# Optimization experiments

Hardware: AMD Instinct MI355X
Metric: run time of the kernel (lower is better)

Reference implementation:

```python
import jax, jax.numpy as jnp
import numpy as np
from jax.scipy.special import logsumexp

B, N_LC, N_TE, D = 4, 2048, 2048, 256
ITERS = 100  # Sinkhorn iterations


def _mlp2(x, W1, b1, W2, b2):
    # 2-layer MLP with ReLU (DETR-style MLP, num_layers=2)
    h = jax.nn.relu(x @ W1.T + b1)
    return h @ W2.T + b2


def _log_optimal_transport(scores, alpha, iters):
    b, m, n = scores.shape
    ms = jnp.float32(m)
    ns = jnp.float32(n)
    # augment score matrix with dustbin row/col -> [b, m+1, n+1]
    bins0 = jnp.broadcast_to(alpha, (b, m, 1))
    bins1 = jnp.broadcast_to(alpha, (b, 1, n))
    binsc = jnp.broadcast_to(alpha, (b, 1, 1))
    Z = jnp.concatenate([
        jnp.concatenate([scores, bins0], axis=-1),
        jnp.concatenate([bins1, binsc], axis=-1)], axis=1)
    norm = -jnp.log(ms + ns)
    log_mu = jnp.concatenate([jnp.full((m,), norm), jnp.log(ns)[None] + norm])
    log_nu = jnp.concatenate([jnp.full((n,), norm), jnp.log(ms)[None] + norm])
    log_mu = jnp.broadcast_to(log_mu[None], (b, m + 1))
    log_nu = jnp.broadcast_to(log_nu[None], (b, n + 1))

    def step(carry, _):
        u, v = carry
        u = log_mu - logsumexp(Z + v[:, None, :], axis=2)
        v = log_nu - logsumexp(Z + u[:, :, None], axis=1)
        return (u, v), None

    u0 = jnp.zeros_like(log_mu)
    v0 = jnp.zeros_like(log_nu)
    (u, v), _ = jax.lax.scan(step, (u0, v0), None, length=iters)
    return Z + u[:, :, None] + v[:, None, :] - norm


def setup_inputs() -> dict:
    key = jax.random.key(0)
    ks = jax.random.split(key, 8)
    s = 1.0 / np.sqrt(D).astype(np.float32)
    return {
        "quer_feat_lc": jax.random.normal(ks[0], (B, N_LC, D), jnp.float32),
        "quer_feat_te": jax.random.normal(ks[1], (B, N_TE, D), jnp.float32),
        "W1_lc": jax.random.normal(ks[2], (D, D), jnp.float32) * s,
        "b1_lc": jnp.zeros((D,), jnp.float32),
        "W2_lc": jax.random.normal(ks[3], (D, D), jnp.float32) * s,
        "b2_lc": jnp.zeros((D,), jnp.float32),
        "W1_te": jax.random.normal(ks[4], (D, D), jnp.float32) * s,
        "b1_te": jnp.zeros((D,), jnp.float32),
        "W2_te": jax.random.normal(ks[5], (D, D), jnp.float32) * s,
        "b2_te": jnp.zeros((D,), jnp.float32),
        "bin_score": jnp.ones((), jnp.float32),
    }


def reference(quer_feat_lc, quer_feat_te, W1_lc, b1_lc, W2_lc, b2_lc,
              W1_te, b1_te, W2_te, b2_te, bin_score):
    f1 = _mlp2(quer_feat_lc, W1_lc, b1_lc, W2_lc, b2_lc)  # [B, N_LC, D]
    f2 = _mlp2(quer_feat_te, W1_te, b1_te, W2_te, b2_te)  # [B, N_TE, D]
    scores = jnp.einsum('bnc,bmc->bnm', f1, f2) / jnp.sqrt(jnp.float32(D))
    Z = _log_optimal_transport(scores, bin_score, ITERS)  # [B, N_LC+1, N_TE+1]
    return jnp.exp(Z)
```

## Files before the change

kernel.cpp:

```cpp
#include <hip/hip_runtime.h>
#include <hip/hip_fp16.h>

#define NQ   2048
#define NB   4
#define DD   256
#define M1   2049
#define STR  2064
#define SINK_ITERS 100
#define PNWG 256
#define PTPB 1024

typedef __attribute__((ext_vector_type(8))) short short8;
typedef __attribute__((ext_vector_type(4))) float floatx4;
typedef __attribute__((ext_vector_type(2))) float floatx2;

__device__ __forceinline__ unsigned short f2bf(float f) {
  unsigned u = __float_as_uint(f);
  u += 0x7FFF + ((u >> 16) & 1);
  return (unsigned short)(u >> 16);
}

__device__ __forceinline__ unsigned char f2fp8(float f) {
  unsigned short u = __half_as_ushort(__float2half(f));
  return (unsigned char)((u + 0x7F + ((u >> 8) & 1)) >> 8);
}

__device__ __forceinline__ int IDX(int j) { return j + (j >> 4); }

__global__ void k_cvt6(const float* __restrict__ x_lc, const float* __restrict__ x_te,
                       const float* __restrict__ w1lc, const float* __restrict__ w2lc,
                       const float* __restrict__ w1te, const float* __restrict__ w2te,
                       unsigned short* __restrict__ Xlc, unsigned short* __restrict__ Xte,
                       unsigned short* __restrict__ Wb) {
  const int NX4 = (NB * NQ * DD) / 4;
  const int NW4 = (DD * DD) / 4;
  int i4 = blockIdx.x * blockDim.x + threadIdx.x;
  const float* src; unsigned short* dst; int off;
  if (i4 < NX4)            { src = x_lc; dst = Xlc; off = i4; }
  else if (i4 < 2 * NX4)   { src = x_te; dst = Xte; off = i4 - NX4; }
  else {
    int k = i4 - 2 * NX4;
    int seg = k / NW4;
    off = k - seg * NW4;
    src = (seg == 0) ? w1lc : (seg == 1) ? w2lc : (seg == 2) ? w1te : w2te;
    dst = Wb + seg * 65536;
  }
  float4 f = ((const float4*)src)[off];
  ushort4 o;
  o.x = f2bf(f.x); o.y = f2bf(f.y); o.z = f2bf(f.z); o.w = f2bf(f.w);
  ((ushort4*)dst)[off] = o;
}

template<int MODE>
__global__ __launch_bounds__(256, 2)
void k_gemm_bt(const unsigned short* __restrict__ A,
               const unsigned short* __restrict__ Bt,
               void* __restrict__ Out, void* __restrict__ Out8,
               const float* __restrict__ bias,
               int K, long aBatch, long bBatch, long oBatch, int ostride)
{
  __shared__ __align__(16) unsigned short lA[128 * 32];
  __shared__ __align__(16) unsigned short lB[128 * 32];
  const int tid  = threadIdx.x;
  const int lane = tid & 63;
  const int w    = tid >> 6;
  const int wm   = (w >> 1) * 64;
  const int wn   = (w & 1) * 64;
  const long bz  = blockIdx.z;
  const unsigned short* Ab = A  + bz * aBatch + (long)blockIdx.y * 128 * K;
  const unsigned short* Bb = Bt + bz * bBatch + (long)blockIdx.x * 128 * K;

  floatx4 acc[4][4];
  #pragma unroll
  for (int i = 0; i < 4; i++)
    #pragma unroll
    for (int j = 0; j < 4; j++) acc[i][j] = (floatx4){0.f, 0.f, 0.f, 0.f};

  for (int kt = 0; kt < K; kt += 32) {
    __syncthreads();
    #pragma unroll
    for (int s0 = 0; s0 < 512; s0 += 256) {
      int s = s0 + tid;
      int row = s >> 2, part = s & 3;
      ((uint4*)lA)[s] = *(const uint4*)(Ab + (long)row * K + kt + part * 8);
      ((uint4*)lB)[s] = *(const uint4*)(Bb + (long)row * K + kt + part * 8);
    }
    __syncthreads();
    const int kq = (lane >> 4) * 8;
    const int rl = lane & 15;
    short8 af[4], bf[4];
    #pragma unroll
    for (int t = 0; t < 4; t++) {
      af[t] = *(const short8*)(lA + (wm + t * 16 + rl) * 32 + kq);
      bf[t] = *(const short8*)(lB + (wn + t * 16 + rl) * 32 + kq);
    }
    #pragma unroll
    for (int i = 0; i < 4; i++)
      #pragma unroll
      for (int j = 0; j < 4; j++)
        acc[i][j] = __builtin_amdgcn_mfma_f32_16x16x32_bf16(af[i], bf[j], acc[i][j], 0, 0, 0);
  }

  const int cl = lane & 15, qd = lane >> 4;
  #pragma unroll
  for (int i = 0; i < 4; i++)
    #pragma unroll
    for (int j = 0; j < 4; j++) {
      const int col = blockIdx.x * 128 + wn + j * 16 + cl;
      const float bcol = (MODE >= 2) ? 0.f : bias[col];
      #pragma unroll
      for (int r = 0; r < 4; r++) {
        const long row = (long)blockIdx.y * 128 + wm + i * 16 + qd * 4 + r;
        float v = acc[i][j][r];
        if (MODE == 0) {
          v += bcol; v = v > 0.f ? v : 0.f;
          ((unsigned short*)Out)[bz * oBatch + row * ostride + col] = f2bf(v);
        } else if (MODE == 1) {
          v += bcol;
          ((unsigned short*)Out)[bz * oBatch + row * ostride + col] = f2bf(v);
        } else {
          v *= 0.0625f;
          v = fminf(fmaxf(v, -15.f), 10.9f);
          float e = __expf(v);
          const long idx = bz * oBatch + row * ostride + col;
          if (MODE == 2) ((__half*)Out)[idx] = __float2half(e);
          ((unsigned char*)Out8)[idx] = f2fp8(e);
        }
      }
    }
}

__global__ void k_fill(__half* __restrict__ E, const float* __restrict__ alphaPtr) {
  const float ea = __expf(*alphaPtr);
  const int idx = blockIdx.x * blockDim.x + threadIdx.x;
  const int n1 = NB * NQ * 16;
  if (idx < n1) {
    int b = idx / (NQ * 16);
    int rr = idx - b * NQ * 16;
    int i = rr >> 4;
    int j = 2048 + (rr & 15);
    E[((long)b * M1 + i) * STR + j] = (j == 2048) ? __float2half(ea) : __float2half(0.f);
  } else {
    int k = idx - n1;
    if (k < NB * STR) {
      int b = k / STR;
      int j = k - b * STR;
      E[((long)b * M1 + 2048) * STR + j] = (j <= 2048) ? __float2half(ea) : __float2half(0.f);
    }
  }
}

__global__ void k_init(float* __restrict__ v, int n, unsigned* __restrict__ bar) {
  int i = blockIdx.x * blockDim.x + threadIdx.x;
  if (i < n) v[i] = 1.0f;
  if (i < 2048) bar[i] = 0u;
}

__device__ __forceinline__ void st_agent(float* p, float v) {
  __hip_atomic_store(p, v, __ATOMIC_RELAXED, __HIP_MEMORY_SCOPE_AGENT);
}
__device__ __forceinline__ float ld_agent(const float* p) {
  return __hip_atomic_load(p, __ATOMIC_RELAXED, __HIP_MEMORY_SCOPE_AGENT);
}
__device__ __forceinline__ unsigned ld_u32_agent(const unsigned* p) {
  return __hip_atomic_load(p, __ATOMIC_RELAXED, __HIP_MEMORY_SCOPE_AGENT);
}

__device__ __forceinline__ float wave_sum(float s) {
  #pragma unroll
  for (int o = 32; o; o >>= 1) s += __shfl_xor(s, o);
  return s;
}

__device__ __forceinline__ float dot16f8(uint4 hv, const float* wp) {
  const unsigned* u = (const unsigned*)&hv;
  float s = 0.f;
#if __has_builtin(__builtin_amdgcn_cvt_pk_f32_bf8)
  #pragma unroll
  for (int q = 0; q < 4; q++) {
    floatx2 lo = __builtin_amdgcn_cvt_pk_f32_bf8((int)u[q], false);
    floatx2 hi = __builtin_amdgcn_cvt_pk_f32_bf8((int)u[q], true);
    s += lo.x * wp[q * 4 + 0] + lo.y * wp[q * 4 + 1]
       + hi.x * wp[q * 4 + 2] + hi.y * wp[q * 4 + 3];
  }
#else
  const unsigned char* p = (const unsigned char*)&hv;
  #pragma unroll
  for (int t = 0; t < 16; t++) {
    unsigned short h = (unsigned short)p[t] << 8;
    s += __half2float(*reinterpret_cast<__half*>(&h)) * wp[t];
  }
#endif
  return s;
}

__global__ __launch_bounds__(PTPB, 4)
void k_sink(const unsigned char* __restrict__ E8, const unsigned char* __restrict__ ET8,
            float* __restrict__ eu, float* __restrict__ ev,
            const float* __restrict__ alphaPtr, unsigned* __restrict__ bar)
{
  __shared__ __align__(16) float sv[2200];
  const int tid  = threadIdx.x;
  const int wg   = blockIdx.x;
  const int b    = wg >> 6;
  const int g    = wg & 63;
  const int wv   = tid >> 6;
  const int lane = tid & 63;
  const int r0   = (g * 16 + wv) * 2;
  const float ea = __expf(alphaPtr[0]);
  const unsigned char* E8r  = E8  + ((long)b * M1 + r0) * STR;
  const unsigned char* ET8r = ET8 + ((long)b * M1 + r0) * STR;
  float* ub = eu + b * STR;
  float* vb = ev + b * STR;
  unsigned* cnt = bar + b * 64;
  unsigned* gen = bar + b * 64 + 32;
  const bool dustwave = (g == 63) && (wv == 15);

  unsigned phase = 0;
  for (int it = 0; it < 2 * SINK_ITERS; ++it) {
    const unsigned char* R = (it & 1) ? ET8r : E8r;
    const float* vin = (it & 1) ? ub : vb;
    float*      vout = (it & 1) ? vb : ub;

    for (int j = tid; j < M1; j += PTPB) sv[IDX(j)] = ld_agent(vin + j);
    __syncthreads();

    uint4 h0c0 = *(const uint4*)(R + lane * 16);
    uint4 h0c1 = *(const uint4*)(R + 1024 + lane * 16);
    uint4 h1c0 = *(const uint4*)(R + STR + lane * 16);
    uint4 h1c1 = *(const uint4*)(R + STR + 1024 + lane * 16);
    const float* w0 = sv + lane * 17;
    const float* w1 = sv + 1088 + lane * 17;
    float a0 = dot16f8(h0c0, w0) + dot16f8(h0c1, w1);
    float a1 = dot16f8(h1c0, w0) + dot16f8(h1c1, w1);
    a0 = wave_sum(a0);
    a1 = wave_sum(a1);
    if (lane == 0) {
      const float wd = ea * sv[IDX(2048)];
      st_agent(vout + r0,     (1.f / 4096.f) / (a0 + wd));
      st_agent(vout + r0 + 1, (1.f / 4096.f) / (a1 + wd));
    }

    if (dustwave) {
      float s = 0.f;
      #pragma unroll
      for (int t = 0; t < 16; t++) s += w0[t] + w1[t];
      s = wave_sum(s);
      if (lane == 0) st_agent(vout + 2048, 0.5f / (ea * (s + sv[IDX(2048)])));
    }

    ++phase;
    __syncthreads();
    if (tid == 0) {
      unsigned old = __hip_atomic_fetch_add(cnt, 1u, __ATOMIC_RELAXED, __HIP_MEMORY_SCOPE_AGENT);
      if (old == phase * 64u - 1u) {
        __hip_atomic_store(gen, phase, __ATOMIC_RELAXED, __HIP_MEMORY_SCOPE_AGENT);
      } else {
        while (ld_u32_agent(gen) < phase)
          __builtin_amdgcn_s_sleep(1);
      }
    }
    __syncthreads();
  }
}

__global__ void k_final(const __half* __restrict__ E, const float* __restrict__ eu,
                        const float* __restrict__ ev, float* __restrict__ out) {
  const int wv = blockIdx.x;
  const int b = wv / M1;
  const int i = wv - b * M1;
  const __half* R = E + ((long)b * M1 + i) * STR;
  const float ui = eu[b * STR + i] * 4096.f;
  const float* evb = ev + b * STR;
  float* orow = out + ((long)b * M1 + i) * M1;
  for (int j = threadIdx.x; j < M1; j += blockDim.x)
    orow[j] = __half2float(R[j]) * ui * evb[j];
}

extern "C" void kernel_launch(void* const* d_in, const int* in_sizes, int n_in,
                              void* d_out, int out_size, void* d_ws, size_t ws_size,
                              hipStream_t stream) {
  const float* x_lc  = (const float*)d_in[0];
  const float* x_te  = (const float*)d_in[1];
  const float* W1_lc = (const float*)d_in[2];
  const float* b1_lc = (const float*)d_in[3];
  const float* W2_lc = (const float*)d_in[4];
  const float* b2_lc = (const float*)d_in[5];
  const float* W1_te = (const float*)d_in[6];
  const float* b1_te = (const float*)d_in[7];
  const float* W2_te = (const float*)d_in[8];
  const float* b2_te = (const float*)d_in[9];
  const float* alpha = (const float*)d_in[10];

  char* ws = (char*)d_ws;
  unsigned short* Xlc = (unsigned short*)(ws + 0);
  unsigned short* Xte = (unsigned short*)(ws + 4194304);
  unsigned short* Wb  = (unsigned short*)(ws + 8388608);
  unsigned short* H   = (unsigned short*)(ws + 8912896);
  unsigned short* F1  = (unsigned short*)(ws + 13107200);
  unsigned short* F2  = (unsigned short*)(ws + 17301504);
  __half* E  = (__half*)(ws + 21495808);
  unsigned char* E8  = (unsigned char*)(ws + 55328896);
  unsigned char* ET8 = (unsigned char*)(ws + 72245440);
  float* eu  = (float*)(ws + 89161984);
  float* ev  = (float*)(ws + 89195008);
  unsigned* bar = (unsigned*)(ws + 89228032);

  k_cvt6<<<4352, 256, 0, stream>>>(x_lc, x_te, W1_lc, W2_lc, W1_te, W2_te,
                                   Xlc, Xte, Wb);

  k_gemm_bt<0><<<dim3(2, 64, 1), 256, 0, stream>>>(Xlc, Wb,          H,  nullptr, b1_lc, DD, 0, 0, 0, DD);
  k_gemm_bt<1><<<dim3(2, 64, 1), 256, 0, stream>>>(H,   Wb + 65536,  F1, nullptr, b2_lc, DD, 0, 0, 0, DD);
  k_gemm_bt<0><<<dim3(2, 64, 1), 256, 0, stream>>>(Xte, Wb + 131072, H,  nullptr, b1_te, DD, 0, 0, 0, DD);
  k_gemm_bt<1><<<dim3(2, 64, 1), 256, 0, stream>>>(H,   Wb + 196608, F2, nullptr, b2_te, DD, 0, 0, 0, DD);

  const long ab = (long)NQ * DD;
  const long ob = (long)M1 * STR;
  k_gemm_bt<2><<<dim3(16, 16, NB), 256, 0, stream>>>(F1, F2, E,  E8,  nullptr, DD, ab, ab, ob, STR);
  k_gemm_bt<3><<<dim3(16, 16, NB), 256, 0, stream>>>(F2, F1, nullptr, ET8, nullptr, DD, ab, ab, ob, STR);

  const int nfill = NB * NQ * 16 + NB * STR;
  k_fill<<<(nfill + 255) / 256, 256, 0, stream>>>(E, alpha);

  k_init<<<(NB * STR + 255) / 256, 256, 0, stream>>>(ev, NB * STR, bar);

  k_sink<<<PNWG, PTPB, 0, stream>>>(E8, ET8, eu, ev, alpha, bar);

  k_final<<<NB * M1, 256, 0, stream>>>(E, eu, ev, (float*)d_out);
}
```

Measured before the change: 971.2 us.

## Use fp16 kernel matrices with packed dot2 in Sinkhorn instead of fp8

The Sinkhorn loop now reads fp16 copies of the exp-score matrix and its transpose instead of fp8 copies. Dot products use packed half-precision fdot2 against a scaled fp16 copy of the scaling vector held in shared memory. This doubles the bytes streamed per iteration but removes the fp8 conversions and improves accuracy. The two MLP layers are also batched into single launches via a z dimension with per-batch bias, and the fill and init kernels are merged to cut launch count.

Result: slower. 1.318 ms (+35.7%).

```diff
diff --git a/kernel.cpp b/kernel.cpp
--- a/kernel.cpp
+++ b/kernel.cpp
@@ -12,20 +12,13 @@
 
 typedef __attribute__((ext_vector_type(8))) short short8;
 typedef __attribute__((ext_vector_type(4))) float floatx4;
-typedef __attribute__((ext_vector_type(2))) float floatx2;
+typedef _Float16 h2 __attribute__((ext_vector_type(2)));
 
 __device__ __forceinline__ unsigned short f2bf(float f) {
   unsigned u = __float_as_uint(f);
   u += 0x7FFF + ((u >> 16) & 1);
   return (unsigned short)(u >> 16);
 }
-
-__device__ __forceinline__ unsigned char f2fp8(float f) {
-  unsigned short u = __half_as_ushort(__float2half(f));
-  return (unsigned char)((u + 0x7F + ((u >> 8) & 1)) >> 8);
-}
-
-__device__ __forceinline__ int IDX(int j) { return j + (j >> 4); }
 
 __global__ void k_cvt6(const float* __restrict__ x_lc, const float* __restrict__ x_te,
                        const float* __restrict__ w1lc, const float* __restrict__ w2lc,
@@ -55,8 +48,8 @@
 __global__ __launch_bounds__(256, 2)
 void k_gemm_bt(const unsigned short* __restrict__ A,
                const unsigned short* __restrict__ Bt,
-               void* __restrict__ Out, void* __restrict__ Out8,
-               const float* __restrict__ bias,
+               void* __restrict__ Out,
+               const float* __restrict__ bias, const float* __restrict__ bias2,
                int K, long aBatch, long bBatch, long oBatch, int ostride)
 {
   __shared__ __align__(16) unsigned short lA[128 * 32];
@@ -69,6 +62,7 @@
   const long bz  = blockIdx.z;
   const unsigned short* Ab = A  + bz * aBatch + (long)blockIdx.y * 128 * K;
   const unsigned short* Bb = Bt + bz * bBatch + (long)blockIdx.x * 128 * K;
+  const float* bp = (bz == 0) ? bias : bias2;
 
   floatx4 acc[4][4];
   #pragma unroll
@@ -107,7 +101,7 @@
     #pragma unroll
     for (int j = 0; j < 4; j++) {
       const int col = blockIdx.x * 128 + wn + j * 16 + cl;
-      const float bcol = (MODE >= 2) ? 0.f : bias[col];
+      const float bcol = (MODE >= 2) ? 0.f : bp[col];
       #pragma unroll
       for (int r = 0; r < 4; r++) {
         const long row = (long)blockIdx.y * 128 + wm + i * 16 + qd * 4 + r;
@@ -121,16 +115,14 @@
         } else {
           v *= 0.0625f;
           v = fminf(fmaxf(v, -15.f), 10.9f);
-          float e = __expf(v);
-          const long idx = bz * oBatch + row * ostride + col;
-          if (MODE == 2) ((__half*)Out)[idx] = __float2half(e);
-          ((unsigned char*)Out8)[idx] = f2fp8(e);
+          ((__half*)Out)[bz * oBatch + row * ostride + col] = __float2half(__expf(v));
         }
       }
     }
 }
 
-__global__ void k_fill(__half* __restrict__ E, const float* __restrict__ alphaPtr) {
+__global__ void k_fillinit(__half* __restrict__ E, const float* __restrict__ alphaPtr,
+                           float* __restrict__ ev, unsigned* __restrict__ bar) {
   const float ea = __expf(*alphaPtr);
   const int idx = blockIdx.x * blockDim.x + threadIdx.x;
   const int n1 = NB * NQ * 16;
@@ -148,12 +140,8 @@
       E[((long)b * M1 + 2048) * STR + j] = (j <= 2048) ? __float2half(ea) : __float2half(0.f);
     }
   }
-}
-
-__global__ void k_init(float* __restrict__ v, int n, unsigned* __restrict__ bar) {
-  int i = blockIdx.x * blockDim.x + threadIdx.x;
-  if (i < n) v[i] = 1.0f;
-  if (i < 2048) bar[i] = 0u;
+  if (idx < NB * STR) ev[idx] = 1.0f;
+  if (idx < 2048) bar[idx] = 0u;
 }
 
 __device__ __forceinline__ void st_agent(float* p, float v) {
@@ -172,34 +160,30 @@
   return s;
 }
 
-__device__ __forceinline__ float dot16f8(uint4 hv, const float* wp) {
-  const unsigned* u = (const unsigned*)&hv;
-  float s = 0.f;
-#if __has_builtin(__builtin_amdgcn_cvt_pk_f32_bf8)
+__device__ __forceinline__ float dot8h(uint4 hv, const h2* wp, float s) {
+  const h2* e = (const h2*)&hv;
+#if __has_builtin(__builtin_amdgcn_fdot2)
+  #pragma unroll
+  for (int q = 0; q < 4; q++)
+    s = __builtin_amdgcn_fdot2(e[q], wp[q], s, false);
+#else
   #pragma unroll
   for (int q = 0; q < 4; q++) {
-    floatx2 lo = __builtin_amdgcn_cvt_pk_f32_bf8((int)u[q], false);
-    floatx2 hi = __builtin_amdgcn_cvt_pk_f32_bf8((int)u[q], true);
-    s += lo.x * wp[q * 4 + 0] + lo.y * wp[q * 4 + 1]
-       + hi.x * wp[q * 4 + 2] + hi.y * wp[q * 4 + 3];
-  }
-#else
-  const unsigned char* p = (const unsigned char*)&hv;
-  #pragma unroll
-  for (int t = 0; t < 16; t++) {
-    unsigned short h = (unsigned short)p[t] << 8;
-    s += __half2float(*reinterpret_cast<__half*>(&h)) * wp[t];
+    float2 a = __half22float2(*(const __half2*)&e[q]);
+    float2 b = __half22float2(*(const __half2*)&wp[q]);
+    s = fmaf(a.x, b.x, fmaf(a.y, b.y, s));
   }
 #endif
   return s;
 }
 
 __global__ __launch_bounds__(PTPB, 4)
-void k_sink(const unsigned char* __restrict__ E8, const unsigned char* __restrict__ ET8,
+void k_sink(const __half* __restrict__ Eh, const __half* __restrict__ ETh,
             float* __restrict__ eu, float* __restrict__ ev,
             const float* __restrict__ alphaPtr, unsigned* __restrict__ bar)
 {
-  __shared__ __align__(16) float sv[2200];
+  __shared__ __align__(16) __half svh[2048];
+  __shared__ float sdust;
   const int tid  = threadIdx.x;
   const int wg   = blockIdx.x;
   const int b    = wg >> 6;
@@ -208,8 +192,8 @@
   const int lane = tid & 63;
   const int r0   = (g * 16 + wv) * 2;
   const float ea = __expf(alphaPtr[0]);
-  const unsigned char* E8r  = E8  + ((long)b * M1 + r0) * STR;
-  const unsigned char* ET8r = ET8 + ((long)b * M1 + r0) * STR;
+  const __half* Er  = Eh  + ((long)b * M1 + r0) * STR;
+  const __half* ETr = ETh + ((long)b * M1 + r0) * STR;
   float* ub = eu + b * STR;
   float* vb = ev + b * STR;
   unsigned* cnt = bar + b * 64;
@@ -218,35 +202,53 @@
 
   unsigned phase = 0;
   for (int it = 0; it < 2 * SINK_ITERS; ++it) {
-    const unsigned char* R = (it & 1) ? ET8r : E8r;
+    const __half* R = (it & 1) ? ETr : Er;
     const float* vin = (it & 1) ? ub : vb;
     float*      vout = (it & 1) ? vb : ub;
 
-    for (int j = tid; j < M1; j += PTPB) sv[IDX(j)] = ld_agent(vin + j);
-    __syncthreads();
-
-    uint4 h0c0 = *(const uint4*)(R + lane * 16);
-    uint4 h0c1 = *(const uint4*)(R + 1024 + lane * 16);
-    uint4 h1c0 = *(const uint4*)(R + STR + lane * 16);
-    uint4 h1c1 = *(const uint4*)(R + STR + 1024 + lane * 16);
-    const float* w0 = sv + lane * 17;
-    const float* w1 = sv + 1088 + lane * 17;
-    float a0 = dot16f8(h0c0, w0) + dot16f8(h0c1, w1);
-    float a1 = dot16f8(h1c0, w0) + dot16f8(h1c1, w1);
+    for (int j = tid; j < 2048; j += PTPB)
+      svh[j] = __float2half(ld_agent(vin + j) * 4096.f);
+    if (tid == 0) sdust = ld_agent(vin + 2048) * 4096.f;
+    __syncthreads();
+
+    uint4 e00 = *(const uint4*)(R +        lane * 16);
+    uint4 e01 = *(const uint4*)(R +        lane * 16 + 8);
+    uint4 e02 = *(const uint4*)(R + 1024 + lane * 16);
+    uint4 e03 = *(const uint4*)(R + 1024 + lane * 16 + 8);
+    uint4 e10 = *(const uint4*)(R + STR  +        lane * 16);
+    uint4 e11 = *(const uint4*)(R + STR  +        lane * 16 + 8);
+    uint4 e12 = *(const uint4*)(R + STR  + 1024 + lane * 16);
+    uint4 e13 = *(const uint4*)(R + STR  + 1024 + lane * 16 + 8);
+    const h2* wp0 = (const h2*)(svh +        lane * 16);
+    const h2* wp1 = (const h2*)(svh + 1024 + lane * 16);
+    float a0 = dot8h(e00, wp0, 0.f);
+    a0 = dot8h(e01, wp0 + 4, a0);
+    a0 = dot8h(e02, wp1, a0);
+    a0 = dot8h(e03, wp1 + 4, a0);
+    float a1 = dot8h(e10, wp0, 0.f);
+    a1 = dot8h(e11, wp0 + 4, a1);
+    a1 = dot8h(e12, wp1, a1);
+    a1 = dot8h(e13, wp1 + 4, a1);
     a0 = wave_sum(a0);
     a1 = wave_sum(a1);
     if (lane == 0) {
-      const float wd = ea * sv[IDX(2048)];
-      st_agent(vout + r0,     (1.f / 4096.f) / (a0 + wd));
-      st_agent(vout + r0 + 1, (1.f / 4096.f) / (a1 + wd));
+      const float wd = ea * sdust;
+      st_agent(vout + r0,     1.f / (a0 + wd));
+      st_agent(vout + r0 + 1, 1.f / (a1 + wd));
     }
 
     if (dustwave) {
       float s = 0.f;
+      const __half2* p0 = (const __half2*)(svh +        lane * 16);
+      const __half2* p1 = (const __half2*)(svh + 1024 + lane * 16);
       #pragma unroll
-      for (int t = 0; t < 16; t++) s += w0[t] + w1[t];
+      for (int q = 0; q < 8; q++) {
+        float2 x = __half22float2(p0[q]);
+        float2 y = __half22float2(p1[q]);
+        s += x.x + x.y + y.x + y.y;
+      }
       s = wave_sum(s);
-      if (lane == 0) st_agent(vout + 2048, 0.5f / (ea * (s + sv[IDX(2048)])));
+      if (lane == 0) st_agent(vout + 2048, 2048.f / (ea * (s + sdust)));
     }
 
     ++phase;
@@ -294,37 +296,36 @@
 
   char* ws = (char*)d_ws;
   unsigned short* Xlc = (unsigned short*)(ws + 0);
-  unsigned short* Xte = (unsigned short*)(ws + 4194304);
   unsigned short* Wb  = (unsigned short*)(ws + 8388608);
   unsigned short* H   = (unsigned short*)(ws + 8912896);
-  unsigned short* F1  = (unsigned short*)(ws + 13107200);
-  unsigned short* F2  = (unsigned short*)(ws + 17301504);
+  unsigned short* F   = (unsigned short*)(ws + 0);
   __half* E  = (__half*)(ws + 21495808);
-  unsigned char* E8  = (unsigned char*)(ws + 55328896);
-  unsigned char* ET8 = (unsigned char*)(ws + 72245440);
+  __half* ET = (__half*)(ws + 55328896);
   float* eu  = (float*)(ws + 89161984);
   float* ev  = (float*)(ws + 89195008);
   unsigned* bar = (unsigned*)(ws + 89228032);
 
+  unsigned short* Xte = Xlc + 2097152;
+
   k_cvt6<<<4352, 256, 0, stream>>>(x_lc, x_te, W1_lc, W2_lc, W1_te, W2_te,
                                    Xlc, Xte, Wb);
 
-  k_gemm_bt<0><<<dim3(2, 64, 1), 256, 0, stream>>>(Xlc, Wb,          H,  nullptr, b1_lc, DD, 0, 0, 0, DD);
-  k_gemm_bt<1><<<dim3(2, 64, 1), 256, 0, stream>>>(H,   Wb + 65536,  F1, nullptr, b2_lc, DD, 0, 0, 0, DD);
-  k_gemm_bt<0><<<dim3(2, 64, 1), 256, 0, stream>>>(Xte, Wb + 131072, H,  nullptr, b1_te, DD, 0, 0, 0, DD);
-  k_gemm_bt<1><<<dim3(2, 64, 1), 256, 0, stream>>>(H,   Wb + 196608, F2, nullptr, b2_te, DD, 0, 0, 0, DD);
-
+  k_gemm_bt<0><<<dim3(2, 64, 2), 256, 0, stream>>>(Xlc, Wb,          H, b1_lc, b1_te,
+                                                   DD, 2097152, 131072, 2097152, DD);
+  k_gemm_bt<1><<<dim3(2, 64, 2), 256, 0, stream>>>(H,   Wb + 65536,  F, b2_lc, b2_te,
+                                                   DD, 2097152, 131072, 2097152, DD);
+
+  unsigned short* F1 = F;
+  unsigned short* F2 = F + 2097152;
   const long ab = (long)NQ * DD;
   const long ob = (long)M1 * STR;
-  k_gemm_bt<2><<<dim3(16, 16, NB), 256, 0, stream>>>(F1, F2, E,  E8,  nullptr, DD, ab, ab, ob, STR);
-  k_gemm_bt<3><<<dim3(16, 16, NB), 256, 0, stream>>>(F2, F1, nullptr, ET8, nullptr, DD, ab, ab, ob, STR);
+  k_gemm_bt<2><<<dim3(16, 16, NB), 256, 0, stream>>>(F1, F2, E,  nullptr, nullptr, DD, ab, ab, ob, STR);
+  k_gemm_bt<2><<<dim3(16, 16, NB), 256, 0, stream>>>(F2, F1, ET, nullptr, nullptr, DD, ab, ab, ob, STR);
 
   const int nfill = NB * NQ * 16 + NB * STR;
-  k_fill<<<(nfill + 255) / 256, 256, 0, stream>>>(E, alpha);
-
-  k_init<<<(NB * STR + 255) / 256, 256, 0, stream>>>(ev, NB * STR, bar);
-
-  k_sink<<<PNWG, PTPB, 0, stream>>>(E8, ET8, eu, ev, alpha, bar);
+  k_fillinit<<<(nfill + 255) / 256, 256, 0, stream>>>(E, alpha, ev, bar);
+
+  k_sink<<<PNWG, PTPB, 0, stream>>>(E, ET, eu, ev, alpha, bar);
 
   k_final<<<NB * M1, 256, 0, stream>>>(E, eu, ev, (float*)d_out);
 }
```

## Cache Sinkhorn rows in LDS, batch MLP GEMMs, merge fill and init kernels

Applied to the files above, without the earlier changes.

Each Sinkhorn wave now loads its two fp8 rows of E and of E^T into a 128KB shared-memory buffer once, before the loop. The 200 iterations then read LDS instead of reissuing global loads every half-step. The two branches of each MLP layer now run as one GEMM launch with a z=2 batch and a per-batch bias pointer, and the workspace is reshuffled so F overwrites the dead X buffers. The fill and init kernels are merged into one launch. The large LDS footprint limits the Sinkhorn kernel to one block per CU, which the persistent grid barrier needs to stay co-resident.

New measurement: 878.1 us. -9.6%, faster.

```diff
diff --git a/kernel.cpp b/kernel.cpp
--- a/kernel.cpp
+++ b/kernel.cpp
@@ -56,7 +56,7 @@
 void k_gemm_bt(const unsigned short* __restrict__ A,
                const unsigned short* __restrict__ Bt,
                void* __restrict__ Out, void* __restrict__ Out8,
-               const float* __restrict__ bias,
+               const float* __restrict__ bias, const float* __restrict__ bias2,
                int K, long aBatch, long bBatch, long oBatch, int ostride)
 {
   __shared__ __align__(16) unsigned short lA[128 * 32];
@@ -69,6 +69,7 @@
   const long bz  = blockIdx.z;
   const unsigned short* Ab = A  + bz * aBatch + (long)blockIdx.y * 128 * K;
   const unsigned short* Bb = Bt + bz * bBatch + (long)blockIdx.x * 128 * K;
+  const float* bp = (bz == 0) ? bias : bias2;
 
   floatx4 acc[4][4];
   #pragma unroll
@@ -107,7 +108,7 @@
     #pragma unroll
     for (int j = 0; j < 4; j++) {
       const int col = blockIdx.x * 128 + wn + j * 16 + cl;
-      const float bcol = (MODE >= 2) ? 0.f : bias[col];
+      const float bcol = (MODE >= 2) ? 0.f : bp[col];
       #pragma unroll
       for (int r = 0; r < 4; r++) {
         const long row = (long)blockIdx.y * 128 + wm + i * 16 + qd * 4 + r;
@@ -130,7 +131,8 @@
     }
 }
 
-__global__ void k_fill(__half* __restrict__ E, const float* __restrict__ alphaPtr) {
+__global__ void k_fillinit(__half* __restrict__ E, const float* __restrict__ alphaPtr,
+                           float* __restrict__ ev, unsigned* __restrict__ bar) {
   const float ea = __expf(*alphaPtr);
   const int idx = blockIdx.x * blockDim.x + threadIdx.x;
   const int n1 = NB * NQ * 16;
@@ -148,12 +150,8 @@
       E[((long)b * M1 + 2048) * STR + j] = (j <= 2048) ? __float2half(ea) : __float2half(0.f);
     }
   }
-}
-
-__global__ void k_init(float* __restrict__ v, int n, unsigned* __restrict__ bar) {
-  int i = blockIdx.x * blockDim.x + threadIdx.x;
-  if (i < n) v[i] = 1.0f;
-  if (i < 2048) bar[i] = 0u;
+  if (idx < NB * STR) ev[idx] = 1.0f;
+  if (idx < 2048) bar[idx] = 0u;
 }
 
 __device__ __forceinline__ void st_agent(float* p, float v) {
@@ -199,6 +197,7 @@
             float* __restrict__ eu, float* __restrict__ ev,
             const float* __restrict__ alphaPtr, unsigned* __restrict__ bar)
 {
+  __shared__ __align__(16) unsigned char rows[131072];
   __shared__ __align__(16) float sv[2200];
   const int tid  = threadIdx.x;
   const int wg   = blockIdx.x;
@@ -216,19 +215,31 @@
   unsigned* gen = bar + b * 64 + 32;
   const bool dustwave = (g == 63) && (wv == 15);
 
+  {
+    uint4* dw = (uint4*)(rows + wv * 8192);
+    dw[lane]       = *(const uint4*)(E8r  +        lane * 16);
+    dw[64 + lane]  = *(const uint4*)(E8r  + 1024 + lane * 16);
+    dw[128 + lane] = *(const uint4*)(E8r  + STR  +        lane * 16);
+    dw[192 + lane] = *(const uint4*)(E8r  + STR  + 1024 + lane * 16);
+    dw[256 + lane] = *(const uint4*)(ET8r +        lane * 16);
+    dw[320 + lane] = *(const uint4*)(ET8r + 1024 + lane * 16);
+    dw[384 + lane] = *(const uint4*)(ET8r + STR  +        lane * 16);
+    dw[448 + lane] = *(const uint4*)(ET8r + STR  + 1024 + lane * 16);
+  }
+
   unsigned phase = 0;
   for (int it = 0; it < 2 * SINK_ITERS; ++it) {
-    const unsigned char* R = (it & 1) ? ET8r : E8r;
     const float* vin = (it & 1) ? ub : vb;
     float*      vout = (it & 1) ? vb : ub;
 
     for (int j = tid; j < M1; j += PTPB) sv[IDX(j)] = ld_agent(vin + j);
     __syncthreads();
 
-    uint4 h0c0 = *(const uint4*)(R + lane * 16);
-    uint4 h0c1 = *(const uint4*)(R + 1024 + lane * 16);
-    uint4 h1c0 = *(const uint4*)(R + STR + lane * 16);
-    uint4 h1c1 = *(const uint4*)(R + STR + 1024 + lane * 16);
+    const unsigned char* Rl = rows + wv * 8192 + ((it & 1) << 12);
+    uint4 h0c0 = *(const uint4*)(Rl +        lane * 16);
+    uint4 h0c1 = *(const uint4*)(Rl + 1024 + lane * 16);
+    uint4 h1c0 = *(const uint4*)(Rl + 2048 + lane * 16);
+    uint4 h1c1 = *(const uint4*)(Rl + 3072 + lane * 16);
     const float* w0 = sv + lane * 17;
     const float* w1 = sv + 1088 + lane * 17;
     float a0 = dot16f8(h0c0, w0) + dot16f8(h0c1, w1);
@@ -294,11 +305,9 @@
 
   char* ws = (char*)d_ws;
   unsigned short* Xlc = (unsigned short*)(ws + 0);
-  unsigned short* Xte = (unsigned short*)(ws + 4194304);
   unsigned short* Wb  = (unsigned short*)(ws + 8388608);
   unsigned short* H   = (unsigned short*)(ws + 8912896);
-  unsigned short* F1  = (unsigned short*)(ws + 13107200);
-  unsigned short* F2  = (unsigned short*)(ws + 17301504);
+  unsigned short* F   = (unsigned short*)(ws + 0);
   __half* E  = (__half*)(ws + 21495808);
   unsigned char* E8  = (unsigned char*)(ws + 55328896);
   unsigned char* ET8 = (unsigned char*)(ws + 72245440);
@@ -306,23 +315,25 @@
   float* ev  = (float*)(ws + 89195008);
   unsigned* bar = (unsigned*)(ws + 89228032);
 
+  unsigned short* Xte = Xlc + 2097152;
+
   k_cvt6<<<4352, 256, 0, stream>>>(x_lc, x_te, W1_lc, W2_lc, W1_te, W2_te,
                                    Xlc, Xte, Wb);
 
-  k_gemm_bt<0><<<dim3(2, 64, 1), 256, 0, stream>>>(Xlc, Wb,          H,  nullptr, b1_lc, DD, 0, 0, 0, DD);
-  k_gemm_bt<1><<<dim3(2, 64, 1), 256, 0, stream>>>(H,   Wb + 65536,  F1, nullptr, b2_lc, DD, 0, 0, 0, DD);
-  k_gemm_bt<0><<<dim3(2, 64, 1), 256, 0, stream>>>(Xte, Wb + 131072, H,  nullptr, b1_te, DD, 0, 0, 0, DD);
-  k_gemm_bt<1><<<dim3(2, 64, 1), 256, 0, stream>>>(H,   Wb + 196608, F2, nullptr, b2_te, DD, 0, 0, 0, DD);
-
+  k_gemm_bt<0><<<dim3(2, 64, 2), 256, 0, stream>>>(Xlc, Wb,         H, nullptr, b1_lc, b1_te,
+                                                   DD, 2097152, 131072, 2097152, DD);
+  k_gemm_bt<1><<<dim3(2, 64, 2), 256, 0, stream>>>(H,   Wb + 65536, F, nullptr, b2_lc, b2_te,
+                                                   DD, 2097152, 131072, 2097152, DD);
+
+  unsigned short* F1 = F;
+  unsigned short* F2 = F + 2097152;
   const long ab = (long)NQ * DD;
   const long ob = (long)M1 * STR;
-  k_gemm_bt<2><<<dim3(16, 16, NB), 256, 0, stream>>>(F1, F2, E,  E8,  nullptr, DD, ab, ab, ob, STR);
-  k_gemm_bt<3><<<dim3(16, 16, NB), 256, 0, stream>>>(F2, F1, nullptr, ET8, nullptr, DD, ab, ab, ob, STR);
+  k_gemm_bt<2><<<dim3(16, 16, NB), 256, 0, stream>>>(F1, F2, E,  E8,  nullptr, nullptr, DD, ab, ab, ob, STR);
+  k_gemm_bt<3><<<dim3(16, 16, NB), 256, 0, stream>>>(F2, F1, nullptr, ET8, nullptr, nullptr, DD, ab, ab, ob, STR);
 
   const int nfill = NB * NQ * 16 + NB * STR;
-  k_fill<<<(nfill + 255) / 256, 256, 0, stream>>>(E, alpha);
-
-  k_init<<<(NB * STR + 255) / 256, 256, 0, stream>>>(ev, NB * STR, bar);
+  k_fillinit<<<(nfill + 255) / 256, 256, 0, stream>>>(E, alpha, ev, bar);
 
   k_sink<<<PNWG, PTPB, 0, stream>>>(E8, ET8, eu, ev, alpha, bar);
 
```
